# Kernel tuning notes

Measured on AMD Instinct MI355X. Metric: run time of the kernel, lower is better.

## Reference

```python
import jax, jax.numpy as jnp
import numpy as np

N_NODES = 100000
N_EDGES = 1600000
N_GRAPHS = 256
D = 32  # node/edge/global feature dim


def setup_inputs() -> dict:
    key = jax.random.key(0)
    k1, k2, k3, k4, k5, k6 = jax.random.split(key, 6)
    x = jax.random.normal(k1, (N_NODES, D), dtype=jnp.float32)
    edge_index = jax.random.randint(k2, (2, N_EDGES), 0, N_NODES, dtype=jnp.int64)
    edge_attr = jax.random.normal(k3, (N_EDGES, D), dtype=jnp.float32)
    u = jax.random.normal(k4, (N_GRAPHS, D), dtype=jnp.float32)
    batch = jnp.sort(jax.random.randint(k5, (N_NODES,), 0, N_GRAPHS, dtype=jnp.int64))
    W = jax.random.normal(k6, (3 * D, D), dtype=jnp.float32) * (1.0 / np.sqrt(3 * D))
    b = jnp.zeros((D,), dtype=jnp.float32)
    return {"x": x, "edge_index": edge_index, "edge_attr": edge_attr,
            "u": u, "batch": batch, "W": W, "b": b}


def reference(x, edge_index, edge_attr, u, batch, W, b):
    src = edge_index[0]
    num_graphs = u.shape[0]
    # scatter-sum node features by graph id
    node_agg = jax.ops.segment_sum(x, batch, num_segments=num_graphs)
    # scatter-sum edge features by graph id of their source node
    edge_agg = jax.ops.segment_sum(edge_attr, batch[src], num_segments=num_graphs)
    global_input = jnp.concatenate([node_agg, edge_agg, u], axis=-1)  # [B, 3D]
    return jax.nn.relu(global_input @ W + b)
```

## Files before the change

### kernel.cpp

```cpp
#include <hip/hip_runtime.h>

#define N_NODES   100000
#define N_EDGES   1600000
#define N_GRAPHS  256
#define D         32
#define GD        (N_GRAPHS * D)
#define LSTRIDE   257
#define NBLK      256
#define NBG       256
#define SCALE_F   1048576.0f
#define INV_SCALE 9.5367431640625e-07f

__global__ __launch_bounds__(1024) void pre_kernel(
        const int* __restrict__ src,
        const int* __restrict__ batch,
        unsigned char* __restrict__ g8,
        const float* __restrict__ x,
        float* __restrict__ npart ) {
    if (blockIdx.x < NBG) {
        const int stride = NBG * 1024;
        int i = blockIdx.x * 1024 + threadIdx.x;
        for (; i + 3 * stride < N_EDGES; i += 4 * stride) {
            const int s0 = src[i];
            const int s1 = src[i + stride];
            const int s2 = src[i + 2 * stride];
            const int s3 = src[i + 3 * stride];
            const int b0 = batch[s0], b1 = batch[s1], b2 = batch[s2], b3 = batch[s3];
            g8[i]              = (unsigned char)b0;
            g8[i + stride]     = (unsigned char)b1;
            g8[i + 2 * stride] = (unsigned char)b2;
            g8[i + 3 * stride] = (unsigned char)b3;
        }
        for (; i < N_EDGES; i += stride) g8[i] = (unsigned char)batch[src[i]];
        return;
    }

    const int g = blockIdx.x - NBG;
    int lo = 0, hi = N_NODES;
    while (lo < hi) { const int m = (lo + hi) >> 1; if (batch[m] < g) lo = m + 1; else hi = m; }
    const int r0 = lo;
    hi = N_NODES;
    while (lo < hi) { const int m = (lo + hi) >> 1; if (batch[m] < g + 1) lo = m + 1; else hi = m; }
    const int r1 = lo;

    const int s = threadIdx.x >> 3;
    const int c = threadIdx.x & 7;
    const float4* __restrict__ x4 = (const float4*)x;

    float4 a = make_float4(0.f, 0.f, 0.f, 0.f);
    for (int r = r0 + s; r < r1; r += 128) {
        const float4 v = x4[r * 8 + c];
        a.x += v.x; a.y += v.y; a.z += v.z; a.w += v.w;
    }

    __shared__ float4 red[1024];
    red[threadIdx.x] = a;
    __syncthreads();
    if (threadIdx.x < 256) {
        float4 t = red[threadIdx.x];
        const float4 b1 = red[threadIdx.x + 256];
        const float4 b2 = red[threadIdx.x + 512];
        const float4 b3 = red[threadIdx.x + 768];
        t.x += b1.x + b2.x + b3.x; t.y += b1.y + b2.y + b3.y;
        t.z += b1.z + b2.z + b3.z; t.w += b1.w + b2.w + b3.w;
        red[threadIdx.x] = t;
    }
    __syncthreads();
    if (threadIdx.x < 8) {
        float4 t = make_float4(0.f, 0.f, 0.f, 0.f);
        #pragma unroll
        for (int s2 = 0; s2 < 32; ++s2) {
            const float4 b = red[s2 * 8 + threadIdx.x];
            t.x += b.x; t.y += b.y; t.z += b.z; t.w += b.w;
        }
        ((float4*)(npart + (size_t)g * D))[threadIdx.x] = t;
    }
}

__global__ __launch_bounds__(1024) void edge_stream_kernel(
        const float* __restrict__ ea,
        const unsigned char* __restrict__ g8,
        int* __restrict__ epart ) {
    __shared__ int lds[D * LSTRIDE];
    for (int i = threadIdx.x; i < D * LSTRIDE; i += 1024) lds[i] = 0;
    __syncthreads();

    const float4* __restrict__ ea4 = (const float4*)ea;
    const int total  = N_EDGES * (D / 4);
    const int stride = gridDim.x * blockDim.x;

    int icur = blockIdx.x * blockDim.x + threadIdx.x;
    bool have = icur < total;
    float4 v = make_float4(0.f, 0.f, 0.f, 0.f);
    int g = 0;
    if (have) { v = ea4[icur]; g = g8[icur >> 3]; }

    while (have) {
        const int inext = icur + stride;
        const bool haven = inext < total;
        float4 vn = make_float4(0.f, 0.f, 0.f, 0.f);
        int gn = 0;
        if (haven) { vn = ea4[inext]; gn = g8[inext >> 3]; }

        const int base = ((icur & 7) * 4) * LSTRIDE + g;
        atomicAdd(&lds[base              ], __float2int_rn(v.x * SCALE_F));
        atomicAdd(&lds[base +     LSTRIDE], __float2int_rn(v.y * SCALE_F));
        atomicAdd(&lds[base + 2 * LSTRIDE], __float2int_rn(v.z * SCALE_F));
        atomicAdd(&lds[base + 3 * LSTRIDE], __float2int_rn(v.w * SCALE_F));

        icur = inext; v = vn; g = gn; have = haven;
    }
    __syncthreads();

    int* __restrict__ my = epart + (size_t)blockIdx.x * GD;
    for (int i = threadIdx.x; i < GD; i += 1024)
        my[i] = lds[(i & 31) * LSTRIDE + (i >> 5)];
}

__global__ __launch_bounds__(256) void finish_kernel(
        const float* __restrict__ npart,
        const int* __restrict__ epart,
        const float* __restrict__ u,
        const float* __restrict__ W,
        const float* __restrict__ bias,
        float* __restrict__ out) {
    const int g = blockIdx.x;
    __shared__ float Ws[3 * D * D];
    __shared__ int   ered[32][33];
    __shared__ float accN[D], accE[D], ush[D];

    for (int i = threadIdx.x; i < 3 * D * D; i += 256) Ws[i] = W[i];

    {
        const int pgrp = threadIdx.x >> 3;
        const int q    = threadIdx.x & 7;
        const int4* __restrict__ ep4 = (const int4*)epart + (size_t)g * 8 + q;
        int4 s4 = make_int4(0, 0, 0, 0);
        for (int p = pgrp; p < NBLK; p += 32) {
            const int4 t = ep4[(size_t)p * (GD / 4)];
            s4.x += t.x; s4.y += t.y; s4.z += t.z; s4.w += t.w;
        }
        ered[pgrp][q * 4 + 0] = s4.x;
        ered[pgrp][q * 4 + 1] = s4.y;
        ered[pgrp][q * 4 + 2] = s4.z;
        ered[pgrp][q * 4 + 3] = s4.w;
    }
    __syncthreads();

    if (threadIdx.x < D) {
        const int d = threadIdx.x;
        int tot = 0;
        #pragma unroll
        for (int pg2 = 0; pg2 < 32; ++pg2) tot += ered[pg2][d];
        accE[d] = (float)tot * INV_SCALE;
        accN[d] = npart[g * D + d];
        ush[d]  = u[g * D + d];
    }
    __syncthreads();

    if (threadIdx.x < D) {
        const int d = threadIdx.x;
        float sacc = bias[d];
        #pragma unroll
        for (int kk = 0; kk < D; ++kk) sacc += accN[kk] * Ws[kk * D + d];
        #pragma unroll
        for (int kk = 0; kk < D; ++kk) sacc += accE[kk] * Ws[(D + kk) * D + d];
        #pragma unroll
        for (int kk = 0; kk < D; ++kk) sacc += ush[kk] * Ws[(2 * D + kk) * D + d];
        out[g * D + d] = fmaxf(sacc, 0.f);
    }
}

extern "C" void kernel_launch(void* const* d_in, const int* in_sizes, int n_in,
                              void* d_out, int out_size, void* d_ws, size_t ws_size,
                              hipStream_t stream) {
    const float* x     = (const float*)d_in[0];
    const int*   ei    = (const int*)  d_in[1];
    const float* ea    = (const float*)d_in[2];
    const float* u     = (const float*)d_in[3];
    const int*   batch = (const int*)  d_in[4];
    const float* W     = (const float*)d_in[5];
    const float* bias  = (const float*)d_in[6];
    float*       out   = (float*)d_out;

    const size_t g8_bytes = (size_t)((N_EDGES + 255) & ~255);
    unsigned char* g8    = (unsigned char*)d_ws;
    float*         npart = (float*)((char*)d_ws + g8_bytes);
    int*           epart = (int*)(npart + GD);

    pre_kernel        <<<NBG + N_GRAPHS, 1024, 0, stream>>>(ei, batch, g8, x, npart);
    edge_stream_kernel<<<NBLK, 1024, 0, stream>>>(ea, g8, epart);
    finish_kernel     <<<N_GRAPHS, 256, 0, stream>>>(npart, epart, u, W, bias, out);
}
```

Measured before the change: 54.41 us.

## Fuse edge graph-id gather into edge stream and node sum into finish kernel

Drops the pre_kernel that built a byte array of per-edge graph ids. The edge stream kernel now looks up batch[src] itself, using a two-deep software pipeline of the src and batch loads. The node segment sum moves into the finish kernel, which runs 1024 threads and reduces the per-block edge partials in two stages. This removes a kernel launch and the g8 write and read pass. In exchange, the edge loop now does a dependent gather per edge element, and the finish kernel carries more per-block work.

Result: faster. 49.73 us (-8.6%).

```diff
diff --git a/kernel.cpp b/kernel.cpp
--- a/kernel.cpp
+++ b/kernel.cpp
@@ -7,35 +7,76 @@
 #define GD        (N_GRAPHS * D)
 #define LSTRIDE   257
 #define NBLK      256
-#define NBG       256
 #define SCALE_F   1048576.0f
 #define INV_SCALE 9.5367431640625e-07f
 
-__global__ __launch_bounds__(1024) void pre_kernel(
+__global__ __launch_bounds__(1024) void edge_stream_kernel(
+        const float* __restrict__ ea,
         const int* __restrict__ src,
         const int* __restrict__ batch,
-        unsigned char* __restrict__ g8,
-        const float* __restrict__ x,
-        float* __restrict__ npart ) {
-    if (blockIdx.x < NBG) {
-        const int stride = NBG * 1024;
-        int i = blockIdx.x * 1024 + threadIdx.x;
-        for (; i + 3 * stride < N_EDGES; i += 4 * stride) {
-            const int s0 = src[i];
-            const int s1 = src[i + stride];
-            const int s2 = src[i + 2 * stride];
-            const int s3 = src[i + 3 * stride];
-            const int b0 = batch[s0], b1 = batch[s1], b2 = batch[s2], b3 = batch[s3];
-            g8[i]              = (unsigned char)b0;
-            g8[i + stride]     = (unsigned char)b1;
-            g8[i + 2 * stride] = (unsigned char)b2;
-            g8[i + 3 * stride] = (unsigned char)b3;
-        }
-        for (; i < N_EDGES; i += stride) g8[i] = (unsigned char)batch[src[i]];
-        return;
+        int* __restrict__ epart ) {
+    __shared__ int lds[D * LSTRIDE];
+    for (int i = threadIdx.x; i < D * LSTRIDE; i += 1024) lds[i] = 0;
+    __syncthreads();
+
+    const float4* __restrict__ ea4 = (const float4*)ea;
+    const int total = N_EDGES * (D / 4);
+    const int S     = NBLK * 1024;
+    const int i0    = blockIdx.x * 1024 + threadIdx.x;
+    const int NIT   = (total + S - 1) / S;
+
+    float4 vA; int gA, sA;
+    {
+        const int ic = min(i0, total - 1);
+        const int st = src[ic >> 3];
+        gA = batch[st];
+        const float4 t = ea4[ic];
+        const float m = (i0 < total) ? 1.f : 0.f;
+        vA = make_float4(t.x * m, t.y * m, t.z * m, t.w * m);
+        sA = src[min(i0 + S, total - 1) >> 3];
     }
 
-    const int g = blockIdx.x - NBG;
+    int i = i0;
+    for (int k = 0; k < NIT; ++k) {
+        const int iS  = i + S;
+        const int sB  = src[min(iS + S, total - 1) >> 3];
+        const int gB  = batch[sA];
+        const float4 tv = ea4[min(iS, total - 1)];
+        const float m = (iS < total) ? 1.f : 0.f;
+        const float4 vB = make_float4(tv.x * m, tv.y * m, tv.z * m, tv.w * m);
+
+        const int base = ((i & 7) * 4) * LSTRIDE + gA;
+        atomicAdd(&lds[base              ], __float2int_rn(vA.x * SCALE_F));
+        atomicAdd(&lds[base +     LSTRIDE], __float2int_rn(vA.y * SCALE_F));
+        atomicAdd(&lds[base + 2 * LSTRIDE], __float2int_rn(vA.z * SCALE_F));
+        atomicAdd(&lds[base + 3 * LSTRIDE], __float2int_rn(vA.w * SCALE_F));
+
+        vA = vB; gA = gB; sA = sB; i = iS;
+    }
+    __syncthreads();
+
+    int* __restrict__ my = epart + (size_t)blockIdx.x * GD;
+    for (int j = threadIdx.x; j < GD; j += 1024)
+        my[j] = lds[(j & 31) * LSTRIDE + (j >> 5)];
+}
+
+__global__ __launch_bounds__(1024) void finish_kernel(
+        const float* __restrict__ x,
+        const int* __restrict__ batch,
+        const int* __restrict__ epart,
+        const float* __restrict__ u,
+        const float* __restrict__ W,
+        const float* __restrict__ bias,
+        float* __restrict__ out) {
+    const int g = blockIdx.x;
+    __shared__ float  Ws[3 * D * D];
+    __shared__ float4 red[1024];
+    __shared__ int4   ered[128][9];
+    __shared__ float  accN[D], accE[D], ush[D];
+
+    for (int j = threadIdx.x; j < 3 * D * D; j += 1024) Ws[j] = W[j];
+    if (threadIdx.x < D) ush[threadIdx.x] = u[g * D + threadIdx.x];
+
     int lo = 0, hi = N_NODES;
     while (lo < hi) { const int m = (lo + hi) >> 1; if (batch[m] < g) lo = m + 1; else hi = m; }
     const int r0 = lo;
@@ -43,19 +84,29 @@
     while (lo < hi) { const int m = (lo + hi) >> 1; if (batch[m] < g + 1) lo = m + 1; else hi = m; }
     const int r1 = lo;
 
-    const int s = threadIdx.x >> 3;
-    const int c = threadIdx.x & 7;
-    const float4* __restrict__ x4 = (const float4*)x;
-
-    float4 a = make_float4(0.f, 0.f, 0.f, 0.f);
-    for (int r = r0 + s; r < r1; r += 128) {
-        const float4 v = x4[r * 8 + c];
-        a.x += v.x; a.y += v.y; a.z += v.z; a.w += v.w;
+    {
+        const int s = threadIdx.x >> 3;
+        const int c = threadIdx.x & 7;
+        const float4* __restrict__ x4 = (const float4*)x;
+        float4 a = make_float4(0.f, 0.f, 0.f, 0.f);
+        for (int r = r0 + s; r < r1; r += 128) {
+            const float4 v = x4[r * 8 + c];
+            a.x += v.x; a.y += v.y; a.z += v.z; a.w += v.w;
+        }
+        red[threadIdx.x] = a;
     }
 
-    __shared__ float4 red[1024];
-    red[threadIdx.x] = a;
+    {
+        const int pg = threadIdx.x >> 3;
+        const int q  = threadIdx.x & 7;
+        const int4* __restrict__ ep4 = (const int4*)epart + (size_t)g * 8 + q;
+        int4 s4 = ep4[(size_t)pg * (GD / 4)];
+        const int4 t4 = ep4[(size_t)(pg + 128) * (GD / 4)];
+        s4.x += t4.x; s4.y += t4.y; s4.z += t4.z; s4.w += t4.w;
+        ered[pg][q] = s4;
+    }
     __syncthreads();
+
     if (threadIdx.x < 256) {
         float4 t = red[threadIdx.x];
         const float4 b1 = red[threadIdx.x + 256];
@@ -64,8 +115,19 @@
         t.x += b1.x + b2.x + b3.x; t.y += b1.y + b2.y + b3.y;
         t.z += b1.z + b2.z + b3.z; t.w += b1.w + b2.w + b3.w;
         red[threadIdx.x] = t;
+    } else if (threadIdx.x < 512) {
+        const int t2 = threadIdx.x - 256;
+        const int j = t2 >> 3, q = t2 & 7;
+        int4 s4 = ered[j][q];
+        const int4 a1 = ered[j + 32][q];
+        const int4 a2 = ered[j + 64][q];
+        const int4 a3 = ered[j + 96][q];
+        s4.x += a1.x + a2.x + a3.x; s4.y += a1.y + a2.y + a3.y;
+        s4.z += a1.z + a2.z + a3.z; s4.w += a1.w + a2.w + a3.w;
+        ered[j][q] = s4;
     }
     __syncthreads();
+
     if (threadIdx.x < 8) {
         float4 t = make_float4(0.f, 0.f, 0.f, 0.f);
         #pragma unroll
@@ -73,88 +135,19 @@
             const float4 b = red[s2 * 8 + threadIdx.x];
             t.x += b.x; t.y += b.y; t.z += b.z; t.w += b.w;
         }
-        ((float4*)(npart + (size_t)g * D))[threadIdx.x] = t;
-    }
-}
-
-__global__ __launch_bounds__(1024) void edge_stream_kernel(
-        const float* __restrict__ ea,
-        const unsigned char* __restrict__ g8,
-        int* __restrict__ epart ) {
-    __shared__ int lds[D * LSTRIDE];
-    for (int i = threadIdx.x; i < D * LSTRIDE; i += 1024) lds[i] = 0;
-    __syncthreads();
-
-    const float4* __restrict__ ea4 = (const float4*)ea;
-    const int total  = N_EDGES * (D / 4);
-    const int stride = gridDim.x * blockDim.x;
-
-    int icur = blockIdx.x * blockDim.x + threadIdx.x;
-    bool have = icur < total;
-    float4 v = make_float4(0.f, 0.f, 0.f, 0.f);
-    int g = 0;
-    if (have) { v = ea4[icur]; g = g8[icur >> 3]; }
-
-    while (have) {
-        const int inext = icur + stride;
-        const bool haven = inext < total;
-        float4 vn = make_float4(0.f, 0.f, 0.f, 0.f);
-        int gn = 0;
-        if (haven) { vn = ea4[inext]; gn = g8[inext >> 3]; }
-
-        const int base = ((icur & 7) * 4) * LSTRIDE + g;
-        atomicAdd(&lds[base              ], __float2int_rn(v.x * SCALE_F));
-        atomicAdd(&lds[base +     LSTRIDE], __float2int_rn(v.y * SCALE_F));
-        atomicAdd(&lds[base + 2 * LSTRIDE], __float2int_rn(v.z * SCALE_F));
-        atomicAdd(&lds[base + 3 * LSTRIDE], __float2int_rn(v.w * SCALE_F));
-
-        icur = inext; v = vn; g = gn; have = haven;
-    }
-    __syncthreads();
-
-    int* __restrict__ my = epart + (size_t)blockIdx.x * GD;
-    for (int i = threadIdx.x; i < GD; i += 1024)
-        my[i] = lds[(i & 31) * LSTRIDE + (i >> 5)];
-}
-
-__global__ __launch_bounds__(256) void finish_kernel(
-        const float* __restrict__ npart,
-        const int* __restrict__ epart,
-        const float* __restrict__ u,
-        const float* __restrict__ W,
-        const float* __restrict__ bias,
-        float* __restrict__ out) {
-    const int g = blockIdx.x;
-    __shared__ float Ws[3 * D * D];
-    __shared__ int   ered[32][33];
-    __shared__ float accN[D], accE[D], ush[D];
-
-    for (int i = threadIdx.x; i < 3 * D * D; i += 256) Ws[i] = W[i];
-
-    {
-        const int pgrp = threadIdx.x >> 3;
-        const int q    = threadIdx.x & 7;
-        const int4* __restrict__ ep4 = (const int4*)epart + (size_t)g * 8 + q;
+        ((float4*)accN)[threadIdx.x] = t;
+    } else if (threadIdx.x < 16) {
+        const int q = threadIdx.x - 8;
         int4 s4 = make_int4(0, 0, 0, 0);
-        for (int p = pgrp; p < NBLK; p += 32) {
-            const int4 t = ep4[(size_t)p * (GD / 4)];
-            s4.x += t.x; s4.y += t.y; s4.z += t.z; s4.w += t.w;
+        #pragma unroll
+        for (int j = 0; j < 32; ++j) {
+            const int4 b = ered[j][q];
+            s4.x += b.x; s4.y += b.y; s4.z += b.z; s4.w += b.w;
         }
-        ered[pgrp][q * 4 + 0] = s4.x;
-        ered[pgrp][q * 4 + 1] = s4.y;
-        ered[pgrp][q * 4 + 2] = s4.z;
-        ered[pgrp][q * 4 + 3] = s4.w;
-    }
-    __syncthreads();
-
-    if (threadIdx.x < D) {
-        const int d = threadIdx.x;
-        int tot = 0;
-        #pragma unroll
-        for (int pg2 = 0; pg2 < 32; ++pg2) tot += ered[pg2][d];
-        accE[d] = (float)tot * INV_SCALE;
-        accN[d] = npart[g * D + d];
-        ush[d]  = u[g * D + d];
+        accE[q * 4 + 0] = (float)s4.x * INV_SCALE;
+        accE[q * 4 + 1] = (float)s4.y * INV_SCALE;
+        accE[q * 4 + 2] = (float)s4.z * INV_SCALE;
+        accE[q * 4 + 3] = (float)s4.w * INV_SCALE;
     }
     __syncthreads();
 
@@ -183,12 +176,8 @@
     const float* bias  = (const float*)d_in[6];
     float*       out   = (float*)d_out;
 
-    const size_t g8_bytes = (size_t)((N_EDGES + 255) & ~255);
-    unsigned char* g8    = (unsigned char*)d_ws;
-    float*         npart = (float*)((char*)d_ws + g8_bytes);
-    int*           epart = (int*)(npart + GD);
+    int* epart = (int*)d_ws;
 
-    pre_kernel        <<<NBG + N_GRAPHS, 1024, 0, stream>>>(ei, batch, g8, x, npart);
-    edge_stream_kernel<<<NBLK, 1024, 0, stream>>>(ea, g8, epart);
-    finish_kernel     <<<N_GRAPHS, 256, 0, stream>>>(npart, epart, u, W, bias, out);
+    edge_stream_kernel<<<NBLK, 1024, 0, stream>>>(ea, ei, batch, epart);
+    finish_kernel     <<<N_GRAPHS, 1024, 0, stream>>>(x, batch, epart, u, W, bias, out);
 }
```
